# Kernel optimization log

Hardware: AMD Instinct MI355X
Metric: run time of the kernel (lower is better)

The kernel has to match this reference:

```python
import math
import jax, jax.numpy as jnp
import numpy as np

IMAGE_SIZE = 224


def _resize_bilinear(img, out_h, out_w):
    """PyTorch F.interpolate(mode='bilinear', align_corners=False) equivalent.
    img: [B, H, W] -> [B, out_h, out_w]. No antialiasing (matches torch default)."""
    B, H, W = img.shape

    def coords(out, size):
        r = jnp.maximum((jnp.arange(out, dtype=jnp.float32) + 0.5) * (size / out) - 0.5, 0.0)
        i0 = jnp.minimum(jnp.floor(r).astype(jnp.int32), size - 1)
        i1 = jnp.minimum(i0 + 1, size - 1)
        w = r - i0.astype(jnp.float32)
        return i0, i1, w

    r0, r1, wr = coords(out_h, H)
    c0, c1, wc = coords(out_w, W)
    rows = img[:, r0, :] * (1.0 - wr)[None, :, None] + img[:, r1, :] * wr[None, :, None]
    out = rows[:, :, c0] * (1.0 - wc)[None, None, :] + rows[:, :, c1] * wc[None, None, :]
    return out


def _normalize_minmax(x, eps=1e-8):
    mn = x.min()
    mx = x.max()
    return jnp.where(mx - mn < eps, jnp.zeros_like(x), (x - mn) / (mx - mn + eps))


def _grid_embed(vals, n):
    """Row-major scatter of vals[:, :n] into a ceil(sqrt(n))^2 grid (zero padded)."""
    B = vals.shape[0]
    gs = int(math.ceil(math.sqrt(n)))
    pad = gs * gs - n
    return jnp.pad(vals, ((0, 0), (0, pad))).reshape(B, gs, gs)


def setup_inputs() -> dict:
    key = jax.random.key(0)
    hidden_state = jax.random.normal(key, (32, 512, 4096, 1), dtype=jnp.float32)
    return {"hidden_state": hidden_state}


def reference(hidden_state):
    B, E, N, _ = hidden_state.shape
    x = hidden_state[..., 0]  # [B, E, N]

    # temporal view: mean over nodes -> [B, E] -> grid -> resize
    t_grid = _grid_embed(x.mean(axis=2), E)
    temporal = _normalize_minmax(_resize_bilinear(t_grid, IMAGE_SIZE, IMAGE_SIZE))

    # spatial view: mean over embedding dim -> [B, N] -> grid -> resize
    s_grid = _grid_embed(x.mean(axis=1), N)
    spatial = _normalize_minmax(_resize_bilinear(s_grid, IMAGE_SIZE, IMAGE_SIZE))

    # correlation view: row-normalized centered features, [B, E, E] correlation
    xc = x - x.mean(axis=2, keepdims=True)
    xn = xc / (jnp.linalg.norm(xc, axis=2, keepdims=True) + 1e-8)
    corr = jnp.einsum('bin,bjn->bij', xn, xn)  # [B, E, E]
    correlation = _normalize_minmax(_resize_bilinear(corr, IMAGE_SIZE, IMAGE_SIZE))

    # [B, 3, image_size, image_size]
    return jnp.stack([temporal, spatial, correlation], axis=1)
```

## Files before the change

### kernel.cpp

```cpp
#include <hip/hip_runtime.h>
#include <hip/hip_bf16.h>
#include <math.h>

#define IMG 224
#define PIX (IMG*IMG)
#define B_ 32
#define E_ 512
#define N_ 4096
#define SV_BLOCKS 256
#define SC_ ((float)(512.0/224.0))
#define RPB 16
#define NCHUNK 32
#define KSPLIT 4
#define KLEN (N_/KSPLIT)
#define NTILE 10

typedef __attribute__((ext_vector_type(8))) short bf16x8;
typedef __attribute__((ext_vector_type(4))) float f32x4;

__device__ inline unsigned short f2bf(float f){
  unsigned u = __float_as_uint(f);
  unsigned r = (u + 0x7FFFu + ((u >> 16) & 1u)) >> 16;
  return (unsigned short)r;
}

__global__ void __launch_bounds__(256) stats_y(const float* __restrict__ x,
                                               float* __restrict__ meanv,
                                               float* __restrict__ colpart,
                                               ushort* __restrict__ y){
  int b = blockIdx.x >> 5, chunk = blockIdx.x & 31;
  int e0 = chunk << 4;
  int t = threadIdx.x;
  __shared__ short sInv[512];
  __shared__ float sW[224];
  __shared__ float red[2][16];
  sInv[t] = -1; sInv[t + 256] = -1;
  __syncthreads();
  if (t < 224){
    float r = fmaxf(((float)t + 0.5f) * SC_ - 0.5f, 0.f);
    int r0 = min((int)r, E_ - 1);
    sW[t] = r - (float)r0;
    sInv[r0] = (short)t;
  }
  __syncthreads();

  float cur[16], prev[16], nxt[16], csum[16];
  #pragma unroll
  for (int j = 0; j < 16; j++){ csum[j] = 0.f; prev[j] = 0.f; }
  const float4* row0 = (const float4*)(x + ((size_t)b * E_ + e0) * N_);
  #pragma unroll
  for (int k = 0; k < 4; k++) *(float4*)(cur + 4 * k) = row0[t + 256 * k];
  float pmu = 0.f, prn = 0.f;

  for (int idx = 0; idx <= RPB; idx++){
    int e = e0 + idx;
    if (e >= E_) break;
    bool hasNext = (idx < RPB) && (e + 1 < E_);
    if (hasNext){
      const float4* nr = (const float4*)(x + ((size_t)b * E_ + e + 1) * N_);
      #pragma unroll
      for (int k = 0; k < 4; k++) *(float4*)(nxt + 4 * k) = nr[t + 256 * k];
    }
    float s = 0.f, ss = 0.f;
    #pragma unroll
    for (int j = 0; j < 16; j++){ s += cur[j]; ss += cur[j] * cur[j]; }
    #pragma unroll
    for (int o = 32; o; o >>= 1){ s += __shfl_down(s, o); ss += __shfl_down(ss, o); }
    int wv = t >> 6, ln = t & 63, p = idx & 1;
    if (ln == 0){ red[p][wv] = s; red[p][8 + wv] = ss; }
    __syncthreads();
    float S  = red[p][0] + red[p][1] + red[p][2] + red[p][3];
    float SS = red[p][8] + red[p][9] + red[p][10] + red[p][11];
    float mu = S * (1.f / N_);
    float var = fmaxf(SS - S * S * (1.f / N_), 0.f);
    float rn = 1.f / (sqrtf(var) + 1e-8f);
    if (idx < RPB){
      #pragma unroll
      for (int j = 0; j < 16; j++) csum[j] += cur[j];
      if (t == 0) meanv[b * E_ + e] = mu;
    }
    if (idx >= 1){
      int i = sInv[e - 1];
      if (i >= 0){
        float w = sW[i];
        float a0 = (1.f - w) * prn, a1 = w * rn;
        float cc = -(a0 * pmu + a1 * mu);
        ushort* yo = y + ((size_t)b * IMG + i) * N_;
        #pragma unroll
        for (int k = 0; k < 4; k++){
          union { ushort u[4]; int2 v; } pk;
          #pragma unroll
          for (int j = 0; j < 4; j++)
            pk.u[j] = f2bf(a0 * prev[4*k+j] + a1 * cur[4*k+j] + cc);
          *(int2*)(yo + 1024 * k + 4 * t) = pk.v;
        }
      }
    }
    pmu = mu; prn = rn;
    #pragma unroll
    for (int j = 0; j < 16; j++){ prev[j] = cur[j]; if (hasNext) cur[j] = nxt[j]; }
  }
  float* cp = colpart + ((size_t)(b * NCHUNK + chunk)) * N_;
  #pragma unroll
  for (int k = 0; k < 4; k++) *(float4*)(cp + 1024 * k + 4 * t) = *(float4*)(csum + 4 * k);
}

__global__ void __launch_bounds__(256) col_finalize(const float* __restrict__ colpart,
                                                    float* __restrict__ colmean){
  int b = blockIdx.x >> 4;
  int n = ((blockIdx.x & 15) << 8) + threadIdx.x;
  float s = 0.f;
  #pragma unroll
  for (int c = 0; c < NCHUNK; c++) s += colpart[((size_t)(b * NCHUNK + c)) * N_ + n];
  colmean[b * N_ + n] = s * (1.f / E_);
}

__device__ inline float grid_val(const float* v, int gs, int n, int r, int c){
  int idx = r * gs + c;
  return (idx < n) ? v[idx] : 0.f;
}
__device__ inline float bilin(const float* v, int gs, int n, int i, int j){
  float sc = (float)((double)gs / 224.0);
  float r = fmaxf(((float)i + 0.5f) * sc - 0.5f, 0.f);
  float c = fmaxf(((float)j + 0.5f) * sc - 0.5f, 0.f);
  int r0 = min((int)r, gs - 1), c0 = min((int)c, gs - 1);
  int r1 = min(r0 + 1, gs - 1), c1 = min(c0 + 1, gs - 1);
  float wr = r - (float)r0, wc = c - (float)c0;
  float v00 = grid_val(v, gs, n, r0, c0), v10 = grid_val(v, gs, n, r1, c0);
  float v01 = grid_val(v, gs, n, r0, c1), v11 = grid_val(v, gs, n, r1, c1);
  float ra = v00 * (1.f - wr) + v10 * wr;
  float rb = v01 * (1.f - wr) + v11 * wr;
  return ra * (1.f - wc) + rb * wc;
}

__global__ void __launch_bounds__(256) small_views(const float* __restrict__ meanv,
                                                   const float* __restrict__ colmean,
                                                   float* __restrict__ out,
                                                   float* __restrict__ scr){
  float tmn = INFINITY, tmx = -INFINITY, smn = INFINITY, smx = -INFINITY;
  for (int g = blockIdx.x * 256 + threadIdx.x; g < B_ * PIX; g += SV_BLOCKS * 256){
    int b = g / PIX, p = g - b * PIX;
    int i = p / IMG, j = p - i * IMG;
    float tv = bilin(meanv   + b * E_, 23, E_, i, j);
    float sv = bilin(colmean + b * N_, 64, N_, i, j);
    out[((size_t)b * 3 + 0) * PIX + p] = tv;
    out[((size_t)b * 3 + 1) * PIX + p] = sv;
    tmn = fminf(tmn, tv); tmx = fmaxf(tmx, tv);
    smn = fminf(smn, sv); smx = fmaxf(smx, sv);
  }
  #pragma unroll
  for (int o = 32; o; o >>= 1){
    tmn = fminf(tmn, __shfl_down(tmn, o)); tmx = fmaxf(tmx, __shfl_down(tmx, o));
    smn = fminf(smn, __shfl_down(smn, o)); smx = fmaxf(smx, __shfl_down(smx, o));
  }
  __shared__ float red[4][4];
  int wv = threadIdx.x >> 6, ln = threadIdx.x & 63;
  if (ln == 0){ red[wv][0] = tmn; red[wv][1] = tmx; red[wv][2] = smn; red[wv][3] = smx; }
  __syncthreads();
  if (threadIdx.x == 0){
    scr[blockIdx.x * 4 + 0] = fminf(fminf(red[0][0], red[1][0]), fminf(red[2][0], red[3][0]));
    scr[blockIdx.x * 4 + 1] = fmaxf(fmaxf(red[0][1], red[1][1]), fmaxf(red[2][1], red[3][1]));
    scr[blockIdx.x * 4 + 2] = fminf(fminf(red[0][2], red[1][2]), fminf(red[2][2], red[3][2]));
    scr[blockIdx.x * 4 + 3] = fmaxf(fmaxf(red[0][3], red[1][3]), fmaxf(red[2][3], red[3][3]));
  }
}

#define LDSTR 72
__device__ const int TI_[NTILE] = {0,0,0,0,1,1,1,2,2,3};
__device__ const int TJ_[NTILE] = {0,1,2,3,1,2,3,2,3,3};

__global__ void __launch_bounds__(256) corr_gemm_sk(const ushort* __restrict__ y,
                                                    float* __restrict__ partials){
  int bt = blockIdx.x % (B_ * NTILE);
  int ks = blockIdx.x / (B_ * NTILE);
  int b = bt / NTILE, tile = bt - b * NTILE;
  int ti = TI_[tile], tj = TJ_[tile];
  const ushort* yb = y + (size_t)b * IMG * N_ + (size_t)ks * KLEN;
  __shared__ ushort lA[64 * LDSTR];
  __shared__ ushort lB[64 * LDSTR];
  int t = threadIdx.x;
  int wv = t >> 6, ln = t & 63;
  int wm = wv & 1, wn = wv >> 1;
  int quad = ln >> 4, l16 = ln & 15;
  f32x4 acc[2][2] = {};
  int s = t & 7, r2 = t >> 3;
  int rA0 = min(ti * 64 + r2,      223), rA1 = min(ti * 64 + r2 + 32, 223);
  int rB0 = min(tj * 64 + r2,      223), rB1 = min(tj * 64 + r2 + 32, 223);
  for (int k0 = 0; k0 < KLEN; k0 += 64){
    int4 a0 = *(const int4*)(yb + (size_t)rA0 * N_ + k0 + s * 8);
    int4 a1 = *(const int4*)(yb + (size_t)rA1 * N_ + k0 + s * 8);
    int4 b0v = *(const int4*)(yb + (size_t)rB0 * N_ + k0 + s * 8);
    int4 b1v = *(const int4*)(yb + (size_t)rB1 * N_ + k0 + s * 8);
    __syncthreads();
    *(int4*)(lA + r2 * LDSTR + s * 8)        = a0;
    *(int4*)(lA + (r2 + 32) * LDSTR + s * 8) = a1;
    *(int4*)(lB + r2 * LDSTR + s * 8)        = b0v;
    *(int4*)(lB + (r2 + 32) * LDSTR + s * 8) = b1v;
    __syncthreads();
    #pragma unroll
    for (int kk = 0; kk < 2; kk++){
      bf16x8 af0 = *(const bf16x8*)(lA + (wm * 32 + l16)      * LDSTR + kk * 32 + quad * 8);
      bf16x8 af1 = *(const bf16x8*)(lA + (wm * 32 + 16 + l16) * LDSTR + kk * 32 + quad * 8);
      bf16x8 bf0 = *(const bf16x8*)(lB + (wn * 32 + l16)      * LDSTR + kk * 32 + quad * 8);
      bf16x8 bf1 = *(const bf16x8*)(lB + (wn * 32 + 16 + l16) * LDSTR + kk * 32 + quad * 8);
      acc[0][0] = __builtin_amdgcn_mfma_f32_16x16x32_bf16(af0, bf0, acc[0][0], 0, 0, 0);
      acc[0][1] = __builtin_amdgcn_mfma_f32_16x16x32_bf16(af0, bf1, acc[0][1], 0, 0, 0);
      acc[1][0] = __builtin_amdgcn_mfma_f32_16x16x32_bf16(af1, bf0, acc[1][0], 0, 0, 0);
      acc[1][1] = __builtin_amdgcn_mfma_f32_16x16x32_bf16(af1, bf1, acc[1][1], 0, 0, 0);
    }
  }
  float* pp = partials + ((size_t)ks * (B_ * NTILE) + bt) * 4096 + t * 16;
  #pragma unroll
  for (int im = 0; im < 2; im++)
    #pragma unroll
    for (int in = 0; in < 2; in++)
      *(f32x4*)(pp + 4 * (im * 2 + in)) = acc[im][in];
}

__global__ void __launch_bounds__(256) corr_reduce(const float* __restrict__ partials,
                                                   float* __restrict__ out,
                                                   float* __restrict__ scr){
  int bt = blockIdx.x;
  int b = bt / NTILE, tile = bt - b * NTILE;
  int ti = TI_[tile], tj = TJ_[tile];
  bool diag = (ti == tj);
  int t = threadIdx.x;
  int wv = t >> 6, ln = t & 63;
  int wm = wv & 1, wn = wv >> 1;
  int quad = ln >> 4, l16 = ln & 15;
  f32x4 acc[2][2];
  #pragma unroll
  for (int im = 0; im < 2; im++)
    #pragma unroll
    for (int in = 0; in < 2; in++){
      f32x4 a = {0.f, 0.f, 0.f, 0.f};
      #pragma unroll
      for (int ks = 0; ks < KSPLIT; ks++)
        a += *(const f32x4*)(partials + ((size_t)ks * (B_ * NTILE) + bt) * 4096
                             + t * 16 + 4 * (im * 2 + in));
      acc[im][in] = a;
    }
  float mn = INFINITY, mx = -INFINITY;
  float* ov = out + ((size_t)b * 3 + 2) * PIX;
  #pragma unroll
  for (int im = 0; im < 2; im++)
    #pragma unroll
    for (int in = 0; in < 2; in++){
      int gi0 = ti * 64 + wm * 32 + im * 16 + quad * 4;
      int gj  = tj * 64 + wn * 32 + in * 16 + l16;
      #pragma unroll
      for (int rg = 0; rg < 4; rg++){
        int gi = gi0 + rg;
        if (gi < IMG && gj < IMG){
          float v = acc[im][in][rg];
          ov[gi * IMG + gj] = v;
          mn = fminf(mn, v); mx = fmaxf(mx, v);
        }
      }
      if (!diag && gj < IMG && gi0 < IMG){
        float4 tv;
        tv.x = acc[im][in][0]; tv.y = acc[im][in][1];
        tv.z = acc[im][in][2]; tv.w = acc[im][in][3];
        *(float4*)(ov + gj * IMG + gi0) = tv;
      }
    }
  #pragma unroll
  for (int o = 32; o; o >>= 1){
    mn = fminf(mn, __shfl_down(mn, o)); mx = fmaxf(mx, __shfl_down(mx, o));
  }
  __shared__ float red[4][2];
  if (ln == 0){ red[wv][0] = mn; red[wv][1] = mx; }
  __syncthreads();
  if (t == 0){
    scr[bt * 2 + 0] = fminf(fminf(red[0][0], red[1][0]), fminf(red[2][0], red[3][0]));
    scr[bt * 2 + 1] = fmaxf(fmaxf(red[0][1], red[1][1]), fmaxf(red[2][1], red[3][1]));
  }
}

__global__ void __launch_bounds__(256) reduce_slots(const float* __restrict__ sv_scr,
                                                    const float* __restrict__ corr_scr,
                                                    float* __restrict__ slots){
  int t = threadIdx.x;
  float tmn = sv_scr[4*t+0], tmx = sv_scr[4*t+1];
  float smn = sv_scr[4*t+2], smx = sv_scr[4*t+3];
  float cmn = INFINITY, cmx = -INFINITY;
  for (int idx = t; idx < B_ * NTILE; idx += 256){
    cmn = fminf(cmn, corr_scr[2*idx]);
    cmx = fmaxf(cmx, corr_scr[2*idx+1]);
  }
  #pragma unroll
  for (int o = 32; o; o >>= 1){
    tmn = fminf(tmn, __shfl_down(tmn, o)); tmx = fmaxf(tmx, __shfl_down(tmx, o));
    smn = fminf(smn, __shfl_down(smn, o)); smx = fmaxf(smx, __shfl_down(smx, o));
    cmn = fminf(cmn, __shfl_down(cmn, o)); cmx = fmaxf(cmx, __shfl_down(cmx, o));
  }
  __shared__ float red[4][6];
  int wv = t >> 6, ln = t & 63;
  if (ln == 0){
    red[wv][0]=tmn; red[wv][1]=tmx; red[wv][2]=smn;
    red[wv][3]=smx; red[wv][4]=cmn; red[wv][5]=cmx;
  }
  __syncthreads();
  if (t == 0){
    slots[0] = fminf(fminf(red[0][0],red[1][0]), fminf(red[2][0],red[3][0]));
    slots[1] = fmaxf(fmaxf(red[0][1],red[1][1]), fmaxf(red[2][1],red[3][1]));
    slots[2] = fminf(fminf(red[0][2],red[1][2]), fminf(red[2][2],red[3][2]));
    slots[3] = fmaxf(fmaxf(red[0][3],red[1][3]), fmaxf(red[2][3],red[3][3]));
    slots[4] = fminf(fminf(red[0][4],red[1][4]), fminf(red[2][4],red[3][4]));
    slots[5] = fmaxf(fmaxf(red[0][5],red[1][5]), fmaxf(red[2][5],red[3][5]));
  }
}

__global__ void __launch_bounds__(256) normalize_k(float* __restrict__ out,
                                                   const float* __restrict__ slots){
  int g = blockIdx.x * 256 + threadIdx.x;
  if (g >= B_ * 3 * PIX) return;
  int view = (g / PIX) % 3;
  float mn = slots[2 * view];
  float mx = slots[2 * view + 1];
  float d = mx - mn;
  float v = out[g];
  out[g] = (d < 1e-8f) ? 0.f : (v - mn) / (d + 1e-8f);
}

extern "C" void kernel_launch(void* const* d_in, const int* in_sizes, int n_in,
                              void* d_out, int out_size, void* d_ws, size_t ws_size,
                              hipStream_t stream){
  const float* x = (const float*)d_in[0];
  float* out = (float*)d_out;
  char* ws = (char*)d_ws;
  float* slots    = (float*)(ws + 0);
  float* meanv    = (float*)(ws + 256);
  float* colmean  = meanv + B_ * E_;
  float* colpart  = colmean + B_ * N_;
  float* sv_scr   = colpart + (size_t)B_ * NCHUNK * N_;
  float* corr_scr = sv_scr + SV_BLOCKS * 4;
  size_t y_off = ((size_t)((char*)(corr_scr + B_ * NTILE * 2) - ws) + 255) & ~(size_t)255;
  ushort* y = (ushort*)(ws + y_off);
  size_t p_off = (y_off + (size_t)B_ * IMG * N_ * 2 + 255) & ~(size_t)255;
  float* partials = (float*)(ws + p_off);

  hipLaunchKernelGGL(stats_y, dim3(B_ * NCHUNK), dim3(256), 0, stream,
                     x, meanv, colpart, y);
  hipLaunchKernelGGL(corr_gemm_sk, dim3(KSPLIT * B_ * NTILE), dim3(256), 0, stream,
                     y, partials);
  hipLaunchKernelGGL(corr_reduce, dim3(B_ * NTILE), dim3(256), 0, stream,
                     partials, out, corr_scr);
  hipLaunchKernelGGL(col_finalize, dim3(B_ * 16), dim3(256), 0, stream,
                     colpart, colmean);
  hipLaunchKernelGGL(small_views, dim3(SV_BLOCKS), dim3(256), 0, stream,
                     meanv, colmean, out, sv_scr);
  hipLaunchKernelGGL(reduce_slots, dim3(1), dim3(256), 0, stream,
                     sv_scr, corr_scr, slots);
  hipLaunchKernelGGL(normalize_k, dim3((B_ * 3 * PIX + 255) / 256), dim3(256), 0, stream,
                     out, slots);
}
```

Before: 449.9 us.

## Fuse column-mean finalize via atomics, remap GEMM blocks per XCD, vectorize normalize

Drops the colpart buffer and the col_finalize kernel by having stats_y atomically add its per-chunk column sums into a zeroed colmean, with the 1/E scale moved into small_views. Remaps corr_gemm_sk block indices so that all split-K and tile blocks of one batch land on the same XCD, aiming for better L2 reuse of y. It also doubles the small_views block count and makes normalize_k process float4 with a precomputed reciprocal. The atomics add contention and make the column sums nondeterministic in order, and a memset launch is added.

```diff
diff --git a/kernel.cpp b/kernel.cpp
--- a/kernel.cpp
+++ b/kernel.cpp
@@ -7,7 +7,7 @@
 #define B_ 32
 #define E_ 512
 #define N_ 4096
-#define SV_BLOCKS 256
+#define SV_BLOCKS 512
 #define SC_ ((float)(512.0/224.0))
 #define RPB 16
 #define NCHUNK 32
@@ -26,7 +26,7 @@
 
 __global__ void __launch_bounds__(256) stats_y(const float* __restrict__ x,
                                                float* __restrict__ meanv,
-                                               float* __restrict__ colpart,
+                                               float* __restrict__ colmean,
                                                ushort* __restrict__ y){
   int b = blockIdx.x >> 5, chunk = blockIdx.x & 31;
   int e0 = chunk << 4;
@@ -100,19 +100,12 @@
     #pragma unroll
     for (int j = 0; j < 16; j++){ prev[j] = cur[j]; if (hasNext) cur[j] = nxt[j]; }
   }
-  float* cp = colpart + ((size_t)(b * NCHUNK + chunk)) * N_;
-  #pragma unroll
-  for (int k = 0; k < 4; k++) *(float4*)(cp + 1024 * k + 4 * t) = *(float4*)(csum + 4 * k);
-}
-
-__global__ void __launch_bounds__(256) col_finalize(const float* __restrict__ colpart,
-                                                    float* __restrict__ colmean){
-  int b = blockIdx.x >> 4;
-  int n = ((blockIdx.x & 15) << 8) + threadIdx.x;
-  float s = 0.f;
-  #pragma unroll
-  for (int c = 0; c < NCHUNK; c++) s += colpart[((size_t)(b * NCHUNK + c)) * N_ + n];
-  colmean[b * N_ + n] = s * (1.f / E_);
+  float* cm = colmean + (size_t)b * N_;
+  #pragma unroll
+  for (int k = 0; k < 4; k++)
+    #pragma unroll
+    for (int j = 0; j < 4; j++)
+      atomicAdd(&cm[1024 * k + 4 * t + j], csum[4 * k + j]);
 }
 
 __device__ inline float grid_val(const float* v, int gs, int n, int r, int c){
@@ -142,7 +135,7 @@
     int b = g / PIX, p = g - b * PIX;
     int i = p / IMG, j = p - i * IMG;
     float tv = bilin(meanv   + b * E_, 23, E_, i, j);
-    float sv = bilin(colmean + b * N_, 64, N_, i, j);
+    float sv = bilin(colmean + b * N_, 64, N_, i, j) * (1.f / E_);
     out[((size_t)b * 3 + 0) * PIX + p] = tv;
     out[((size_t)b * 3 + 1) * PIX + p] = sv;
     tmn = fminf(tmn, tv); tmx = fmaxf(tmx, tv);
@@ -171,9 +164,13 @@
 
 __global__ void __launch_bounds__(256) corr_gemm_sk(const ushort* __restrict__ y,
                                                     float* __restrict__ partials){
-  int bt = blockIdx.x % (B_ * NTILE);
-  int ks = blockIdx.x / (B_ * NTILE);
-  int b = bt / NTILE, tile = bt - b * NTILE;
+  int xcd  = blockIdx.x & 7;
+  int slot = blockIdx.x >> 3;
+  int b    = (xcd << 2) + (slot / 40);
+  int rem  = slot % 40;
+  int ks   = rem / 10;
+  int tile = rem - ks * 10;
+  int bt   = b * NTILE + tile;
   int ti = TI_[tile], tj = TJ_[tile];
   const ushort* yb = y + (size_t)b * IMG * N_ + (size_t)ks * KLEN;
   __shared__ ushort lA[64 * LDSTR];
@@ -281,8 +278,11 @@
                                                     const float* __restrict__ corr_scr,
                                                     float* __restrict__ slots){
   int t = threadIdx.x;
-  float tmn = sv_scr[4*t+0], tmx = sv_scr[4*t+1];
-  float smn = sv_scr[4*t+2], smx = sv_scr[4*t+3];
+  float tmn = INFINITY, tmx = -INFINITY, smn = INFINITY, smx = -INFINITY;
+  for (int i = t; i < SV_BLOCKS; i += 256){
+    tmn = fminf(tmn, sv_scr[4*i+0]); tmx = fmaxf(tmx, sv_scr[4*i+1]);
+    smn = fminf(smn, sv_scr[4*i+2]); smx = fmaxf(smx, sv_scr[4*i+3]);
+  }
   float cmn = INFINITY, cmx = -INFINITY;
   for (int idx = t; idx < B_ * NTILE; idx += 256){
     cmn = fminf(cmn, corr_scr[2*idx]);
@@ -314,13 +314,20 @@
 __global__ void __launch_bounds__(256) normalize_k(float* __restrict__ out,
                                                    const float* __restrict__ slots){
   int g = blockIdx.x * 256 + threadIdx.x;
-  if (g >= B_ * 3 * PIX) return;
-  int view = (g / PIX) % 3;
+  int base = g * 4;
+  if (base >= B_ * 3 * PIX) return;
+  int view = (base / PIX) % 3;
   float mn = slots[2 * view];
   float mx = slots[2 * view + 1];
   float d = mx - mn;
-  float v = out[g];
-  out[g] = (d < 1e-8f) ? 0.f : (v - mn) / (d + 1e-8f);
+  float inv = 1.f / (d + 1e-8f);
+  bool z = d < 1e-8f;
+  float4 v = *(float4*)(out + base);
+  v.x = z ? 0.f : (v.x - mn) * inv;
+  v.y = z ? 0.f : (v.y - mn) * inv;
+  v.z = z ? 0.f : (v.z - mn) * inv;
+  v.w = z ? 0.f : (v.w - mn) * inv;
+  *(float4*)(out + base) = v;
 }
 
 extern "C" void kernel_launch(void* const* d_in, const int* in_sizes, int n_in,
@@ -332,26 +339,24 @@
   float* slots    = (float*)(ws + 0);
   float* meanv    = (float*)(ws + 256);
   float* colmean  = meanv + B_ * E_;
-  float* colpart  = colmean + B_ * N_;
-  float* sv_scr   = colpart + (size_t)B_ * NCHUNK * N_;
+  float* sv_scr   = colmean + B_ * N_;
   float* corr_scr = sv_scr + SV_BLOCKS * 4;
   size_t y_off = ((size_t)((char*)(corr_scr + B_ * NTILE * 2) - ws) + 255) & ~(size_t)255;
   ushort* y = (ushort*)(ws + y_off);
   size_t p_off = (y_off + (size_t)B_ * IMG * N_ * 2 + 255) & ~(size_t)255;
   float* partials = (float*)(ws + p_off);
 
+  hipMemsetAsync(colmean, 0, (size_t)B_ * N_ * sizeof(float), stream);
   hipLaunchKernelGGL(stats_y, dim3(B_ * NCHUNK), dim3(256), 0, stream,
-                     x, meanv, colpart, y);
+                     x, meanv, colmean, y);
   hipLaunchKernelGGL(corr_gemm_sk, dim3(KSPLIT * B_ * NTILE), dim3(256), 0, stream,
                      y, partials);
   hipLaunchKernelGGL(corr_reduce, dim3(B_ * NTILE), dim3(256), 0, stream,
                      partials, out, corr_scr);
-  hipLaunchKernelGGL(col_finalize, dim3(B_ * 16), dim3(256), 0, stream,
-                     colpart, colmean);
   hipLaunchKernelGGL(small_views, dim3(SV_BLOCKS), dim3(256), 0, stream,
                      meanv, colmean, out, sv_scr);
   hipLaunchKernelGGL(reduce_slots, dim3(1), dim3(256), 0, stream,
                      sv_scr, corr_scr, slots);
-  hipLaunchKernelGGL(normalize_k, dim3((B_ * 3 * PIX + 255) / 256), dim3(256), 0, stream,
+  hipLaunchKernelGGL(normalize_k, dim3((B_ * 3 * PIX / 4 + 255) / 256), dim3(256), 0, stream,
                      out, slots);
 }
```

New measurement: 463.3 us. +3.0%, slower.
